# Optimization experiments

Measured on AMD Instinct MI355X. Metric: run time of the kernel, lower is better.

## Reference

```python
import jax, jax.numpy as jnp
import numpy as np

N_SRC = 100000
N_DST = 100000
N_EDGES = 1600000
IN_FEATS = 256
HEADS = 4
D_OUT = 64
NEG_SLOPE = 0.2


def setup_inputs() -> dict:
    key = jax.random.key(0)
    ks = jax.random.split(key, 7)
    return {
        "feat_src": jax.random.normal(ks[0], (N_SRC, IN_FEATS), dtype=jnp.float32),
        "feat_dst": jax.random.normal(ks[1], (N_DST, IN_FEATS), dtype=jnp.float32),
        "edge_src": jax.random.randint(ks[2], (N_EDGES,), 0, N_SRC, dtype=jnp.int32),
        "edge_dst": jax.random.randint(ks[3], (N_EDGES,), 0, N_DST, dtype=jnp.int32),
        "W": jax.random.normal(ks[4], (IN_FEATS, HEADS * D_OUT), dtype=jnp.float32) * 0.06,
        "attn_l": jax.random.normal(ks[5], (HEADS, D_OUT), dtype=jnp.float32) * 0.1,
        "attn_r": jax.random.normal(ks[6], (HEADS, D_OUT), dtype=jnp.float32) * 0.1,
    }


def reference(feat_src, feat_dst, edge_src, edge_dst, W, attn_l, attn_r):
    # fc projection (no bias), reshape to [N, H, D]
    fsrc = (feat_src @ W).reshape(-1, HEADS, D_OUT)
    fdst = (feat_dst @ W).reshape(-1, HEADS, D_OUT)
    # per-node attention logits: el [N_src, H], er [N_dst, H]
    el = jnp.einsum('nhd,hd->nh', fsrc, attn_l)
    er = jnp.einsum('nhd,hd->nh', fdst, attn_r)
    # per-edge logit = leaky_relu(el[src] + er[dst]); original uses raw exp (no max-sub)
    e = el[edge_src] + er[edge_dst]                          # [E, H]
    e = jnp.where(e >= 0, e, NEG_SLOPE * e)
    s = jnp.exp(e)                                           # [E, H]
    # edge softmax denominator: segment sum over dst nodes
    out_sum = jax.ops.segment_sum(s, edge_dst, num_segments=N_DST)  # [N_dst, H]
    a = s / out_sum[edge_dst]                                # [E, H]
    # weighted neighbor aggregation: m = ft[src] * a, summed per dst
    m = fsrc[edge_src] * a[:, :, None]                       # [E, H, D]
    rst = jax.ops.segment_sum(m, edge_dst, num_segments=N_DST)      # [N_dst, H, D]
    return rst
```

## Files before the change

kernel.cpp:

```cpp
#include <hip/hip_runtime.h>
#include <hip/hip_bf16.h>
#include <math.h>

#define N_SRC   100000
#define N_DST   100000
#define N_EDGES 1600000
#define IN_F    256
#define HEADS   4
#define D_OUT   64
#define NHD     256
#define NEG_SLOPE 0.2f

typedef __attribute__((ext_vector_type(8))) short          bf16x8;
typedef __attribute__((ext_vector_type(8))) unsigned short u16x8;
typedef __attribute__((ext_vector_type(4))) float          f32x4;

__device__ inline void split_bf16(float x, unsigned short& h, unsigned short& l) {
    unsigned u = __float_as_uint(x);
    unsigned uh = u + (0x7fffu + ((u >> 16) & 1u));
    h = (unsigned short)(uh >> 16);
    float hf = __uint_as_float(uh & 0xffff0000u);
    float r = x - hf;
    unsigned ur = __float_as_uint(r);
    l = (unsigned short)((ur + (0x7fffu + ((ur >> 16) & 1u))) >> 16);
}

__global__ void k_wr(const float* __restrict__ W, const float* __restrict__ ar,
                     float* __restrict__ wr) {
    __shared__ float a[NHD];
    int t = threadIdx.x;
    a[t] = ar[t];
    __syncthreads();
    float s[HEADS] = {0.f, 0.f, 0.f, 0.f};
    for (int h = 0; h < HEADS; ++h) {
        float acc = 0.f;
        #pragma unroll 8
        for (int d = 0; d < D_OUT; ++d)
            acc += W[t * NHD + h * D_OUT + d] * a[h * D_OUT + d];
        s[h] = acc;
    }
    *(float4*)&wr[t * 4] = make_float4(s[0], s[1], s[2], s[3]);
}

__global__ void k_wcast(const float* __restrict__ W,
                        unsigned short* __restrict__ Wht,
                        unsigned short* __restrict__ Wlt) {
    int n = blockIdx.x;
    int k = threadIdx.x;
    float x = W[k * NHD + n];
    unsigned short h, l;
    split_bf16(x, h, l);
    Wht[n * IN_F + k] = h;
    Wlt[n * IN_F + k] = l;
}

__global__ __launch_bounds__(256) void k_er(const float* __restrict__ fdst,
                                            const float* __restrict__ wr,
                                            float* __restrict__ er) {
    __shared__ float4 wrs[256];
    int t = threadIdx.x;
    wrs[t] = ((const float4*)wr)[t];
    __syncthreads();
    int node = blockIdx.x * 4 + (t >> 6);
    int lane = t & 63;
    float4 f = *(const float4*)&fdst[(size_t)node * IN_F + lane * 4];
    float4 w0 = wrs[lane * 4 + 0], w1 = wrs[lane * 4 + 1];
    float4 w2 = wrs[lane * 4 + 2], w3 = wrs[lane * 4 + 3];
    float px = f.x * w0.x + f.y * w1.x + f.z * w2.x + f.w * w3.x;
    float py = f.x * w0.y + f.y * w1.y + f.z * w2.y + f.w * w3.y;
    float pz = f.x * w0.z + f.y * w1.z + f.z * w2.z + f.w * w3.z;
    float pw = f.x * w0.w + f.y * w1.w + f.z * w2.w + f.w * w3.w;
    #pragma unroll
    for (int m = 1; m < 64; m <<= 1) {
        px += __shfl_xor(px, m);
        py += __shfl_xor(py, m);
        pz += __shfl_xor(pz, m);
        pw += __shfl_xor(pw, m);
    }
    if (lane == 0)
        *(float4*)&er[node * 4] = make_float4(px, py, pz, pw);
}

#define GBM 128
#define GBK 32
__global__ __launch_bounds__(512, 2) void k_gemm_mfma(
        const float* __restrict__ A, const unsigned short* __restrict__ Bht,
        const unsigned short* __restrict__ Blt, const float* __restrict__ al_g,
        float* __restrict__ C, float* __restrict__ el) {
    __shared__ __align__(16) unsigned short Ah[GBM][GBK], Al[GBM][GBK];
    __shared__ __align__(16) unsigned short Bh[NHD][GBK], Bl[NHD][GBK];
    const int t = threadIdx.x;
    const int m0 = blockIdx.x * GBM;
    const int wid = t >> 6, lane = t & 63;
    const int wm = wid >> 2, wn = wid & 3;
    const int fr = lane & 15, fq = lane >> 4;
    const int kb = fq * 8;

    f32x4 acc[4][4];
    #pragma unroll
    for (int m = 0; m < 4; ++m)
        #pragma unroll
        for (int n = 0; n < 4; ++n)
            acc[m][n] = (f32x4){0.f, 0.f, 0.f, 0.f};

    const int ar = t >> 2, ac = (t & 3) * 8;
    const bool avalid = (m0 + ar) < N_SRC;
    const float* aptr = A + (size_t)(m0 + ar) * IN_F + ac;
    const int bn = t >> 1, bk = (t & 1) * 16;

    for (int k0 = 0; k0 < IN_F; k0 += GBK) {
        float4 v0 = make_float4(0.f, 0.f, 0.f, 0.f), v1 = v0;
        if (avalid) {
            v0 = *(const float4*)(aptr + k0);
            v1 = *(const float4*)(aptr + k0 + 4);
        }
        u16x8 bh0 = *(const u16x8*)(Bht + (size_t)bn * IN_F + k0 + bk);
        u16x8 bh1 = *(const u16x8*)(Bht + (size_t)bn * IN_F + k0 + bk + 8);
        u16x8 bl0 = *(const u16x8*)(Blt + (size_t)bn * IN_F + k0 + bk);
        u16x8 bl1 = *(const u16x8*)(Blt + (size_t)bn * IN_F + k0 + bk + 8);
        float xs[8] = {v0.x, v0.y, v0.z, v0.w, v1.x, v1.y, v1.z, v1.w};
        u16x8 hv, lv;
        #pragma unroll
        for (int j = 0; j < 8; ++j) {
            unsigned short hh, ll;
            split_bf16(xs[j], hh, ll);
            hv[j] = hh; lv[j] = ll;
        }
        __syncthreads();
        *(u16x8*)&Ah[ar][ac] = hv;
        *(u16x8*)&Al[ar][ac] = lv;
        *(u16x8*)&Bh[bn][bk]     = bh0;
        *(u16x8*)&Bh[bn][bk + 8] = bh1;
        *(u16x8*)&Bl[bn][bk]     = bl0;
        *(u16x8*)&Bl[bn][bk + 8] = bl1;
        __syncthreads();
        bf16x8 afh[4], afl[4], bfh[4], bfl[4];
        #pragma unroll
        for (int m = 0; m < 4; ++m) {
            afh[m] = *(const bf16x8*)&Ah[wm * 64 + m * 16 + fr][kb];
            afl[m] = *(const bf16x8*)&Al[wm * 64 + m * 16 + fr][kb];
        }
        #pragma unroll
        for (int n = 0; n < 4; ++n) {
            bfh[n] = *(const bf16x8*)&Bh[wn * 64 + n * 16 + fr][kb];
            bfl[n] = *(const bf16x8*)&Bl[wn * 64 + n * 16 + fr][kb];
        }
        #pragma unroll
        for (int m = 0; m < 4; ++m)
            #pragma unroll
            for (int n = 0; n < 4; ++n) {
                acc[m][n] = __builtin_amdgcn_mfma_f32_16x16x32_bf16(afh[m], bfh[n], acc[m][n], 0, 0, 0);
                acc[m][n] = __builtin_amdgcn_mfma_f32_16x16x32_bf16(afh[m], bfl[n], acc[m][n], 0, 0, 0);
                acc[m][n] = __builtin_amdgcn_mfma_f32_16x16x32_bf16(afl[m], bfh[n], acc[m][n], 0, 0, 0);
            }
    }

    float alw[4];
    #pragma unroll
    for (int n = 0; n < 4; ++n) alw[n] = al_g[wn * 64 + n * 16 + fr];
    #pragma unroll
    for (int m = 0; m < 4; ++m) {
        int rbase = m0 + wm * 64 + m * 16 + fq * 4;
        float elp[4] = {0.f, 0.f, 0.f, 0.f};
        #pragma unroll
        for (int n = 0; n < 4; ++n) {
            f32x4 a = acc[m][n];
            int col = wn * 64 + n * 16 + fr;
            float w = alw[n];
            elp[0] += a[0] * w; elp[1] += a[1] * w;
            elp[2] += a[2] * w; elp[3] += a[3] * w;
            #pragma unroll
            for (int j = 0; j < 4; ++j)
                if (rbase + j < N_SRC)
                    C[(size_t)(rbase + j) * NHD + col] = a[j];
        }
        #pragma unroll
        for (int j = 0; j < 4; ++j) {
            float s = elp[j];
            s += __shfl_xor(s, 1); s += __shfl_xor(s, 2);
            s += __shfl_xor(s, 4); s += __shfl_xor(s, 8);
            if (fr == 0 && rbase + j < N_SRC)
                el[(rbase + j) * HEADS + wn] = s;
        }
    }
}

__global__ void k_hist(const int* __restrict__ edst, int* __restrict__ deg) {
    int e = blockIdx.x * 256 + threadIdx.x;
    if (e < N_EDGES) atomicAdd(&deg[edst[e]], 1);
}

#define SCAN_B 1024
__global__ __launch_bounds__(SCAN_B) void k_scanA(const int* __restrict__ deg,
                                                  int* __restrict__ off,
                                                  int* __restrict__ bsum) {
    int t = threadIdx.x, b = blockIdx.x;
    int i = b * SCAN_B + t;
    int v = (i < N_DST) ? deg[i] : 0;
    int incl = v;
    int lane = t & 63, w = t >> 6;
    #pragma unroll
    for (int d = 1; d < 64; d <<= 1) {
        int u = __shfl_up(incl, d);
        if (lane >= d) incl += u;
    }
    __shared__ int ws[16];
    if (lane == 63) ws[w] = incl;
    __syncthreads();
    if (t == 0) {
        int run = 0;
        for (int j = 0; j < 16; ++j) { int x = ws[j]; ws[j] = run; run += x; }
        bsum[b] = run;
    }
    __syncthreads();
    if (i < N_DST) off[i] = incl - v + ws[w];
}

__global__ void k_scanB(int* __restrict__ bsum, int nb) {
    if (threadIdx.x == 0 && blockIdx.x == 0) {
        int run = 0;
        for (int j = 0; j < nb; ++j) { int x = bsum[j]; bsum[j] = run; run += x; }
    }
}

__global__ __launch_bounds__(SCAN_B) void k_scanC(int* __restrict__ off,
                                                  const int* __restrict__ bsum) {
    int t = threadIdx.x, b = blockIdx.x;
    int i = b * SCAN_B + t;
    if (i < N_DST) off[i] += bsum[b];
    if (i == 0) off[N_DST] = N_EDGES;
}

__global__ void k_scatter(const int* __restrict__ esrc, const int* __restrict__ edst,
                          const float* __restrict__ el, const float* __restrict__ er,
                          const int* __restrict__ off, int* __restrict__ cursor,
                          int* __restrict__ ssrc, float4* __restrict__ ss) {
    int e = blockIdx.x * 256 + threadIdx.x;
    if (e >= N_EDGES) return;
    int src = esrc[e], dst = edst[e];
    float4 l4 = *(const float4*)&el[src * 4];
    float4 r4 = *(const float4*)&er[dst * 4];
    float ex = l4.x + r4.x, ey = l4.y + r4.y, ez = l4.z + r4.z, ew = l4.w + r4.w;
    ex = (ex >= 0.f) ? ex : NEG_SLOPE * ex;
    ey = (ey >= 0.f) ? ey : NEG_SLOPE * ey;
    ez = (ez >= 0.f) ? ez : NEG_SLOPE * ez;
    ew = (ew >= 0.f) ? ew : NEG_SLOPE * ew;
    float4 s = make_float4(expf(ex), expf(ey), expf(ez), expf(ew));
    int pos = off[dst] + atomicAdd(&cursor[dst], 1);
    ssrc[pos] = src;
    ss[pos] = s;
}

__global__ __launch_bounds__(256) void k_agg(const int* __restrict__ off,
                                             const int* __restrict__ ssrc,
                                             const float* __restrict__ ss,
                                             const float* __restrict__ fsrc,
                                             float* __restrict__ out) {
    int b = blockIdx.x;
    int t = threadIdx.x;
    int s0 = off[b], s1 = off[b + 1];
    int w = t >> 6, lane = t & 63;
    int h = lane >> 4;
    int col = lane << 2;

    __shared__ float inv_den[HEADS];
    __shared__ float red[4][NHD];

    if (t < 64) {
        int hh = t & 3;
        float p = 0.f;
        for (int i = s0 + (t >> 2); i < s1; i += 16)
            p += ss[(size_t)i * 4 + hh];
        #pragma unroll
        for (int m = 4; m < 64; m <<= 1) p += __shfl_xor(p, m);
        if (t < 4) inv_den[t] = (p > 0.f) ? (1.0f / p) : 0.f;
    }

    float4 acc = make_float4(0.f, 0.f, 0.f, 0.f);
    int i = s0 + w;
    for (; i + 4 < s1; i += 8) {
        int   srcA = ssrc[i];
        int   srcB = ssrc[i + 4];
        float aA = ss[(size_t)i * 4 + h];
        float aB = ss[(size_t)(i + 4) * 4 + h];
        float4 fA = *(const float4*)&fsrc[(size_t)srcA * NHD + col];
        float4 fB = *(const float4*)&fsrc[(size_t)srcB * NHD + col];
        acc.x += aA * fA.x; acc.y += aA * fA.y;
        acc.z += aA * fA.z; acc.w += aA * fA.w;
        acc.x += aB * fB.x; acc.y += aB * fB.y;
        acc.z += aB * fB.z; acc.w += aB * fB.w;
    }
    if (i < s1) {
        int   src = ssrc[i];
        float a   = ss[(size_t)i * 4 + h];
        float4 f  = *(const float4*)&fsrc[(size_t)src * NHD + col];
        acc.x += a * f.x; acc.y += a * f.y;
        acc.z += a * f.z; acc.w += a * f.w;
    }
    *(float4*)&red[w][col] = acc;
    __syncthreads();

    float r = red[0][t] + red[1][t] + red[2][t] + red[3][t];
    out[(size_t)b * NHD + t] = r * inv_den[t >> 6];
}

extern "C" void kernel_launch(void* const* d_in, const int* in_sizes, int n_in,
                              void* d_out, int out_size, void* d_ws, size_t ws_size,
                              hipStream_t stream) {
    const float* feat_src = (const float*)d_in[0];
    const float* feat_dst = (const float*)d_in[1];
    const int*   edge_src = (const int*)d_in[2];
    const int*   edge_dst = (const int*)d_in[3];
    const float* W        = (const float*)d_in[4];
    const float* attn_l   = (const float*)d_in[5];
    const float* attn_r   = (const float*)d_in[6];
    float* out = (float*)d_out;

    char* base = (char*)d_ws;
    float* fsrc     = (float*)(base);
    float* sorted_s = (float*)(base + 102400000);
    unsigned short* Wht = (unsigned short*)(base + 102400000);
    unsigned short* Wlt = (unsigned short*)(base + 102400000 + 131072);
    float* el       = (float*)(base + 128000000);
    float* er       = (float*)(base + 129600000);
    float* wr       = (float*)(base + 131200000);
    int*   deg      = (int*)  (base + 131204096);
    int*   off      = (int*)  (base + 131604096);
    int*   cursor   = (int*)  (base + 132004112);
    int*   bsum     = (int*)  (base + 132404112);
    int*   ssrc     = (int*)  (base + 132404624);

    hipMemsetAsync(deg, 0, N_DST * sizeof(int), stream);
    hipMemsetAsync(cursor, 0, N_DST * sizeof(int), stream);

    k_wr<<<1, 256, 0, stream>>>(W, attn_r, wr);
    k_wcast<<<256, 256, 0, stream>>>(W, Wht, Wlt);
    k_er<<<N_DST / 4, 256, 0, stream>>>(feat_dst, wr, er);
    int gblocks = (N_SRC + GBM - 1) / GBM;
    k_gemm_mfma<<<gblocks, 512, 0, stream>>>(feat_src, Wht, Wlt, attn_l, fsrc, el);
    k_hist<<<(N_EDGES + 255) / 256, 256, 0, stream>>>(edge_dst, deg);
    int nb = (N_DST + SCAN_B - 1) / SCAN_B;
    k_scanA<<<nb, SCAN_B, 0, stream>>>(deg, off, bsum);
    k_scanB<<<1, 64, 0, stream>>>(bsum, nb);
    k_scanC<<<nb, SCAN_B, 0, stream>>>(off, bsum);
    k_scatter<<<(N_EDGES + 255) / 256, 256, 0, stream>>>(
        edge_src, edge_dst, el, er, off, cursor, ssrc, (float4*)sorted_s);
    k_agg<<<N_DST, 256, 0, stream>>>(off, ssrc, sorted_s, fsrc, out);
}
```

Before: 726.4 us.

## Recompute edge scores on the fly and split aggregation into column halves

The scatter pass no longer computes or stores per-edge exp scores. A new per-destination kernel computes the softmax denominators from el/er, and the aggregation kernel recomputes each edge's score inline. Aggregation now runs as two launches, each covering 128 of the 256 feature columns, so each pass reads a smaller fsrc working set that should fit better in cache. The cost is extra exp work and el reads, repeated in each pass, plus one more launch.

```diff
diff --git a/kernel.cpp b/kernel.cpp
--- a/kernel.cpp
+++ b/kernel.cpp
@@ -232,76 +232,106 @@
 }
 
 __global__ void k_scatter(const int* __restrict__ esrc, const int* __restrict__ edst,
-                          const float* __restrict__ el, const float* __restrict__ er,
                           const int* __restrict__ off, int* __restrict__ cursor,
-                          int* __restrict__ ssrc, float4* __restrict__ ss) {
+                          int* __restrict__ ssrc) {
     int e = blockIdx.x * 256 + threadIdx.x;
     if (e >= N_EDGES) return;
     int src = esrc[e], dst = edst[e];
-    float4 l4 = *(const float4*)&el[src * 4];
-    float4 r4 = *(const float4*)&er[dst * 4];
-    float ex = l4.x + r4.x, ey = l4.y + r4.y, ez = l4.z + r4.z, ew = l4.w + r4.w;
-    ex = (ex >= 0.f) ? ex : NEG_SLOPE * ex;
-    ey = (ey >= 0.f) ? ey : NEG_SLOPE * ey;
-    ez = (ez >= 0.f) ? ez : NEG_SLOPE * ez;
-    ew = (ew >= 0.f) ? ew : NEG_SLOPE * ew;
-    float4 s = make_float4(expf(ex), expf(ey), expf(ez), expf(ew));
     int pos = off[dst] + atomicAdd(&cursor[dst], 1);
     ssrc[pos] = src;
-    ss[pos] = s;
+}
+
+__global__ __launch_bounds__(256) void k_denom(const int* __restrict__ off,
+                                               const int* __restrict__ ssrc,
+                                               const float* __restrict__ el,
+                                               const float* __restrict__ er,
+                                               float* __restrict__ inv_den) {
+    int n = blockIdx.x * 4 + (threadIdx.x >> 6);
+    int lane = threadIdx.x & 63;
+    int s0 = off[n], s1 = off[n + 1];
+    float4 r4 = *(const float4*)&er[n * 4];
+    float4 p = make_float4(0.f, 0.f, 0.f, 0.f);
+    for (int i = s0 + lane; i < s1; i += 64) {
+        int src = ssrc[i];
+        float4 l4 = *(const float4*)&el[src * 4];
+        float ex = l4.x + r4.x, ey = l4.y + r4.y;
+        float ez = l4.z + r4.z, ew = l4.w + r4.w;
+        ex = (ex >= 0.f) ? ex : NEG_SLOPE * ex;
+        ey = (ey >= 0.f) ? ey : NEG_SLOPE * ey;
+        ez = (ez >= 0.f) ? ez : NEG_SLOPE * ez;
+        ew = (ew >= 0.f) ? ew : NEG_SLOPE * ew;
+        p.x += __expf(ex); p.y += __expf(ey);
+        p.z += __expf(ez); p.w += __expf(ew);
+    }
+    #pragma unroll
+    for (int m = 1; m < 64; m <<= 1) {
+        p.x += __shfl_xor(p.x, m);
+        p.y += __shfl_xor(p.y, m);
+        p.z += __shfl_xor(p.z, m);
+        p.w += __shfl_xor(p.w, m);
+    }
+    if (lane == 0) {
+        float4 inv;
+        inv.x = (p.x > 0.f) ? 1.0f / p.x : 0.f;
+        inv.y = (p.y > 0.f) ? 1.0f / p.y : 0.f;
+        inv.z = (p.z > 0.f) ? 1.0f / p.z : 0.f;
+        inv.w = (p.w > 0.f) ? 1.0f / p.w : 0.f;
+        *(float4*)&inv_den[n * 4] = inv;
+    }
 }
 
 __global__ __launch_bounds__(256) void k_agg(const int* __restrict__ off,
                                              const int* __restrict__ ssrc,
-                                             const float* __restrict__ ss,
+                                             const float* __restrict__ el,
+                                             const float* __restrict__ er,
+                                             const float* __restrict__ inv_den,
                                              const float* __restrict__ fsrc,
-                                             float* __restrict__ out) {
+                                             float* __restrict__ out, int p) {
     int b = blockIdx.x;
     int t = threadIdx.x;
     int s0 = off[b], s1 = off[b + 1];
-    int w = t >> 6, lane = t & 63;
-    int h = lane >> 4;
-    int col = lane << 2;
-
-    __shared__ float inv_den[HEADS];
-    __shared__ float red[4][NHD];
-
-    if (t < 64) {
-        int hh = t & 3;
-        float p = 0.f;
-        for (int i = s0 + (t >> 2); i < s1; i += 16)
-            p += ss[(size_t)i * 4 + hh];
-        #pragma unroll
-        for (int m = 4; m < 64; m <<= 1) p += __shfl_xor(p, m);
-        if (t < 4) inv_den[t] = (p > 0.f) ? (1.0f / p) : 0.f;
-    }
+    int ws = t >> 5;
+    int sl = t & 31;
+    int c  = p * 128 + sl * 4;
+    int h  = c >> 6;
+    float erh = er[b * 4 + h];
+
+    __shared__ float red[8][128];
 
     float4 acc = make_float4(0.f, 0.f, 0.f, 0.f);
-    int i = s0 + w;
-    for (; i + 4 < s1; i += 8) {
-        int   srcA = ssrc[i];
-        int   srcB = ssrc[i + 4];
-        float aA = ss[(size_t)i * 4 + h];
-        float aB = ss[(size_t)(i + 4) * 4 + h];
-        float4 fA = *(const float4*)&fsrc[(size_t)srcA * NHD + col];
-        float4 fB = *(const float4*)&fsrc[(size_t)srcB * NHD + col];
+    int i = s0 + ws;
+    for (; i + 8 < s1; i += 16) {
+        int srcA = ssrc[i], srcB = ssrc[i + 8];
+        float eA = el[srcA * 4 + h] + erh;
+        float eB = el[srcB * 4 + h] + erh;
+        eA = (eA >= 0.f) ? eA : NEG_SLOPE * eA;
+        eB = (eB >= 0.f) ? eB : NEG_SLOPE * eB;
+        float aA = __expf(eA), aB = __expf(eB);
+        float4 fA = *(const float4*)&fsrc[(size_t)srcA * NHD + c];
+        float4 fB = *(const float4*)&fsrc[(size_t)srcB * NHD + c];
         acc.x += aA * fA.x; acc.y += aA * fA.y;
         acc.z += aA * fA.z; acc.w += aA * fA.w;
         acc.x += aB * fB.x; acc.y += aB * fB.y;
         acc.z += aB * fB.z; acc.w += aB * fB.w;
     }
     if (i < s1) {
-        int   src = ssrc[i];
-        float a   = ss[(size_t)i * 4 + h];
-        float4 f  = *(const float4*)&fsrc[(size_t)src * NHD + col];
+        int src = ssrc[i];
+        float e = el[src * 4 + h] + erh;
+        e = (e >= 0.f) ? e : NEG_SLOPE * e;
+        float a = __expf(e);
+        float4 f = *(const float4*)&fsrc[(size_t)src * NHD + c];
         acc.x += a * f.x; acc.y += a * f.y;
         acc.z += a * f.z; acc.w += a * f.w;
     }
-    *(float4*)&red[w][col] = acc;
-    __syncthreads();
-
-    float r = red[0][t] + red[1][t] + red[2][t] + red[3][t];
-    out[(size_t)b * NHD + t] = r * inv_den[t >> 6];
+    *(float4*)&red[ws][sl * 4] = acc;
+    __syncthreads();
+
+    if (t < 128) {
+        float r = red[0][t] + red[1][t] + red[2][t] + red[3][t]
+                + red[4][t] + red[5][t] + red[6][t] + red[7][t];
+        int col = p * 128 + t;
+        out[(size_t)b * NHD + col] = r * inv_den[b * 4 + (col >> 6)];
+    }
 }
 
 extern "C" void kernel_launch(void* const* d_in, const int* in_sizes, int n_in,
@@ -318,9 +348,9 @@
 
     char* base = (char*)d_ws;
     float* fsrc     = (float*)(base);
-    float* sorted_s = (float*)(base + 102400000);
     unsigned short* Wht = (unsigned short*)(base + 102400000);
     unsigned short* Wlt = (unsigned short*)(base + 102400000 + 131072);
+    float* inv_den  = (float*)(base + 103000000);
     float* el       = (float*)(base + 128000000);
     float* er       = (float*)(base + 129600000);
     float* wr       = (float*)(base + 131200000);
@@ -344,6 +374,8 @@
     k_scanB<<<1, 64, 0, stream>>>(bsum, nb);
     k_scanC<<<nb, SCAN_B, 0, stream>>>(off, bsum);
     k_scatter<<<(N_EDGES + 255) / 256, 256, 0, stream>>>(
-        edge_src, edge_dst, el, er, off, cursor, ssrc, (float4*)sorted_s);
-    k_agg<<<N_DST, 256, 0, stream>>>(off, ssrc, sorted_s, fsrc, out);
-}
+        edge_src, edge_dst, off, cursor, ssrc);
+    k_denom<<<N_DST / 4, 256, 0, stream>>>(off, ssrc, el, er, inv_den);
+    k_agg<<<N_DST, 256, 0, stream>>>(off, ssrc, el, er, inv_den, fsrc, out, 0);
+    k_agg<<<N_DST, 256, 0, stream>>>(off, ssrc, el, er, inv_den, fsrc, out, 1);
+}
```

New measurement: 780.4 us. 1.07x slower.
